# Kernel tuning notes

Measured on AMD Instinct MI355X. Metric: run time of the kernel, lower is better.

Reference implementation:

```python
import jax, jax.numpy as jnp
import numpy as np

N, E = 100000, 1600000
D_IN, D_H, D_OUT = 128, 256, 64


def _linear_params(k, fin, fout):
    b = 1.0 / np.sqrt(fin)
    k1, k2 = jax.random.split(k)
    W = jax.random.uniform(k1, (fout, fin), minval=-b, maxval=b, dtype=jnp.float32)
    bias = jax.random.uniform(k2, (fout,), minval=-b, maxval=b, dtype=jnp.float32)
    return W, bias


def setup_inputs() -> dict:
    key = jax.random.key(0)
    ks = jax.random.split(key, 10)
    x = jax.random.normal(ks[0], (N, D_IN), dtype=jnp.float32)
    row = jax.random.randint(ks[1], (E,), 0, N)
    col = jax.random.randint(ks[2], (E,), 0, N)
    vals = jax.random.uniform(ks[3], (E,), dtype=jnp.float32)
    W1a, b1a = _linear_params(ks[4], D_IN, D_H)
    W2a, b2a = _linear_params(ks[5], D_H, D_H)
    W1b, b1b = _linear_params(ks[6], D_H, D_H)
    W2b, b2b = _linear_params(ks[7], D_H, D_H)
    Wf1, bf1 = _linear_params(ks[8], D_H, D_H)
    Wf2, bf2 = _linear_params(ks[9], D_H, D_OUT)
    eps0 = jnp.zeros((1,), jnp.float32)
    eps1 = jnp.zeros((1,), jnp.float32)
    return {"x": x, "row": row, "col": col, "vals": vals,
            "eps0": eps0, "W1a": W1a, "b1a": b1a, "W2a": W2a, "b2a": b2a,
            "eps1": eps1, "W1b": W1b, "b1b": b1b, "W2b": W2b, "b2b": b2b,
            "Wf1": Wf1, "bf1": bf1, "Wf2": Wf2, "bf2": bf2}


def _spmm(row, col, vals, x):
    # y[i] = sum_j A[i,j] * x[j] over edges (row=i, col=j)
    msg = vals[:, None] * x[col]          # [E, d] gather
    return jax.ops.segment_sum(msg, row, num_segments=N)  # [N, d] scatter-add


def _gin_conv(x, row, col, vals, eps, W1, b1, W2, b2):
    y = _spmm(row, col, vals, x)
    h = y + (1.0 + eps) * x               # eps-residual (eps shape [1] broadcasts)
    h = jax.nn.relu(h @ W1.T + b1)
    return h @ W2.T + b2


def reference(x, row, col, vals, eps0, W1a, b1a, W2a, b2a,
              eps1, W1b, b1b, W2b, b2b, Wf1, bf1, Wf2, bf2):
    h = _gin_conv(x, row, col, vals, eps0, W1a, b1a, W2a, b2a)
    h = _gin_conv(h, row, col, vals, eps1, W1b, b1b, W2b, b2b)
    h = jax.nn.relu(h @ Wf1.T + bf1)
    # F.dropout with p=0 (default forward arg) is identity
    return h @ Wf2.T + bf2
```

## Files before the change

### kernel.cpp

```cpp
#include <hip/hip_runtime.h>
#include <cstdint>
#include <cstddef>


using h8  = __attribute__((ext_vector_type(8))) _Float16;
using us8 = __attribute__((ext_vector_type(8))) unsigned short;
using f4  = __attribute__((ext_vector_type(4))) float;

__device__ inline unsigned short f2h(float f) {
    _Float16 h = (_Float16)f;
    unsigned short u;
    __builtin_memcpy(&u, &h, 2);
    return u;
}

__device__ inline void wprep_body(const float* __restrict__ W,
                                  unsigned short* __restrict__ Wf,
                                  int K, int M, int idx) {
    int group = idx >> 9;
    int r     = idx & 511;
    int lane  = r >> 3;
    int j     = r & 7;
    int c  = group / (M / 16);
    int ct = group - c * (M / 16);
    int n = ct * 16 + (lane & 15);
    int k = c * 32 + (lane >> 4) * 8 + j;
    float w = W[(size_t)n * K + k];
    Wf[(size_t)group * 512 + (size_t)lane * 8 + j] = f2h(w);
}

__global__ __launch_bounds__(256) void k_prep0(
        const float* __restrict__ x, unsigned short* __restrict__ xh,
        int* __restrict__ cnt, int N, int ncv, int nzb,
        const float* W1a, unsigned short* Q1a, const float* W2a, unsigned short* Q2a,
        const float* W1b, unsigned short* Q1b, const float* W2b, unsigned short* Q2b,
        const float* Wf1, unsigned short* Qf1, const float* Wf2, unsigned short* Qf2) {
    int b = blockIdx.x;
    if (b < ncv) {
        int i = (b * 256 + threadIdx.x) * 4;
        float4 v = *(const float4*)(x + i);
        ushort4 o = {f2h(v.x), f2h(v.y), f2h(v.z), f2h(v.w)};
        *(ushort4*)(xh + i) = o;
        return;
    }
    b -= ncv;
    if (b < nzb) {
        int i = b * 256 + threadIdx.x;
        if (i < N) cnt[i] = 0;
        return;
    }
    b -= nzb;
    const float* W; unsigned short* Q; int K, M, lb;
    if      (b < 128)  { W = W1a; Q = Q1a; K = 128; M = 256; lb = b; }
    else if (b < 384)  { W = W2a; Q = Q2a; K = 256; M = 256; lb = b - 128; }
    else if (b < 640)  { W = W1b; Q = Q1b; K = 256; M = 256; lb = b - 384; }
    else if (b < 896)  { W = W2b; Q = Q2b; K = 256; M = 256; lb = b - 640; }
    else if (b < 1152) { W = Wf1; Q = Qf1; K = 256; M = 256; lb = b - 896; }
    else               { W = Wf2; Q = Qf2; K = 256; M = 64;  lb = b - 1152; }
    wprep_body(W, Q, K, M, lb * 256 + threadIdx.x);
}

__global__ __launch_bounds__(256) void k_scatter_d(const int* __restrict__ row,
                                                   const int* __restrict__ col,
                                                   const float* __restrict__ vals,
                                                   int* __restrict__ cnt,
                                                   int2* __restrict__ edges, int E) {
    int e = blockIdx.x * 256 + threadIdx.x;
    if (e < E) {
        int r = row[e];
        int p = atomicAdd(&cnt[r], 1);
        if (p < 64)
            edges[(size_t)r * 64 + p] = make_int2(col[e], __float_as_int(vals[e]));
    }
}

template <int DIN>
__device__ inline void gather_phase(const int* __restrict__ cnt,
                                    const int2* __restrict__ edges,
                                    const unsigned short* __restrict__ Xh,
                                    unsigned short* __restrict__ S,
                                    float scale, int r0, int wq, int lane,
                                    int lm, int N) {
    constexpr int L = DIN / 8;
    constexpr int R = 64 / L;
    constexpr int U = 8 / R;
    const int sub  = lane % L;
    const int part = lane / L;

    int nb = r0 + wq * 16 + lm;
    int cv = 0;
    if (nb < N) { cv = cnt[nb]; cv = cv < 64 ? cv : 64; }

    for (int j = 0; j < 16; ++j) {
        int n = r0 + wq * 16 + j;
        float acc[8];
#pragma unroll
        for (int k = 0; k < 8; ++k) acc[k] = 0.0f;
        bool valid = (n < N);
        if (valid) {
            int rem = __shfl(cv, j);
            if (rem > 0) {
                int s = n * 64;
                int idx = s + (lane < rem ? lane : 0);
                int2 ed = edges[idx];
                int   ci = ed.x;
                float vi = (lane < rem) ? __int_as_float(ed.y) : 0.0f;
                for (int jj = 0; jj < rem; jj += 8) {
                    int cc[U]; float vv[U];
#pragma unroll
                    for (int u = 0; u < U; ++u) {
                        int sl = jj + u * R + part;
                        cc[u] = __shfl(ci, sl);
                        vv[u] = __shfl(vi, sl);
                    }
                    h8 g[U];
#pragma unroll
                    for (int u = 0; u < U; ++u)
                        g[u] = *(const h8*)(Xh + (size_t)cc[u] * DIN + sub * 8);
#pragma unroll
                    for (int u = 0; u < U; ++u)
#pragma unroll
                        for (int k = 0; k < 8; ++k)
                            acc[k] = fmaf((float)g[u][k], vv[u], acc[k]);
                }
            }
#pragma unroll
            for (int st = L; st < 64; st <<= 1)
#pragma unroll
                for (int k = 0; k < 8; ++k)
                    acc[k] += __shfl_xor(acc[k], st);
        }
        if (part == 0) {
            us8 o;
            if (valid) {
                h8 xs = *(const h8*)(Xh + (size_t)n * DIN + sub * 8);
#pragma unroll
                for (int k = 0; k < 8; ++k)
                    o[k] = f2h(acc[k] + scale * (float)xs[k]);
            } else {
#pragma unroll
                for (int k = 0; k < 8; ++k) o[k] = 0;
            }
            int c = sub >> 2, q = sub & 3;
            unsigned off = (unsigned)(c * 2048 + wq * 512 + q * 128
                                      + ((j ^ (sub & 7)) * 8));
            *(us8*)(S + off) = o;
        }
    }
}

template <int DIN>
__global__ __launch_bounds__(256, 3) void k_conv(const int* __restrict__ cnt,
                                                 const int2* __restrict__ edges,
                                                 const unsigned short* __restrict__ Xh,
                                                 const unsigned short* __restrict__ Wq1,
                                                 const float* __restrict__ b1,
                                                 const unsigned short* __restrict__ Wq2,
                                                 const float* __restrict__ b2,
                                                 unsigned short* __restrict__ Cout,
                                                 const float* __restrict__ epsp,
                                                 int N) {
    constexpr int MH   = 256;
    constexpr int RT   = 4;
    constexpr int NCT1 = MH / 64;
    constexpr int NCH1 = DIN / 32;
    constexpr int NCH2 = MH / 32;
    constexpr int NCT2 = MH / 64;
    constexpr int HS   = 264;
    __shared__ unsigned short S[64 * HS];

    const int t    = threadIdx.x;
    const int lane = t & 63;
    const int wq   = t >> 6;
    const int r0   = blockIdx.x * 64;
    const int lm   = lane & 15;
    const int lq   = lane >> 4;
    const int kq   = lq * 8;

    const unsigned short* w1b = Wq1 + (size_t)(wq * NCT1) * 512 + (size_t)lane * 8;
    h8 wv[NCT1], wvn[NCT1];
#pragma unroll
    for (int ct = 0; ct < NCT1; ++ct)
        wv[ct] = *(const h8*)(w1b + ct * 512);

    gather_phase<DIN>(cnt, edges, Xh, S, 1.0f + epsp[0], r0, wq, lane, lm, N);
    __syncthreads();

    f4 acc[RT][NCT1];
#pragma unroll
    for (int rt = 0; rt < RT; ++rt)
#pragma unroll
        for (int ct = 0; ct < NCT1; ++ct) acc[rt][ct] = (f4){0.f, 0.f, 0.f, 0.f};

#pragma unroll
    for (int c = 0; c < NCH1; ++c) {
        if (c + 1 < NCH1) {
#pragma unroll
            for (int ct = 0; ct < NCT1; ++ct)
                wvn[ct] = *(const h8*)(w1b + ((size_t)(c + 1) * (MH / 16) + ct) * 512);
        }
        const int key = (4 * c + lq) & 7;
        h8 ah[RT];
#pragma unroll
        for (int rt = 0; rt < RT; ++rt)
            ah[rt] = *(const h8*)(S + c * 2048 + rt * 512 + lq * 128 + (lm ^ key) * 8);
#pragma unroll
        for (int ct = 0; ct < NCT1; ++ct)
#pragma unroll
            for (int rt = 0; rt < RT; ++rt)
                acc[rt][ct] = __builtin_amdgcn_mfma_f32_16x16x32_f16(ah[rt], wv[ct], acc[rt][ct], 0, 0, 0);
        if (c + 1 < NCH1) {
#pragma unroll
            for (int ct = 0; ct < NCT1; ++ct) wv[ct] = wvn[ct];
        }
    }
    __syncthreads();

#pragma unroll
    for (int ct = 0; ct < NCT1; ++ct) {
        const int col = wq * 64 + ct * 16 + lm;
        const float bv = b1[col];
#pragma unroll
        for (int rt = 0; rt < RT; ++rt) {
#pragma unroll
            for (int reg = 0; reg < 4; ++reg) {
                int rrow = rt * 16 + lq * 4 + reg;
                float v = acc[rt][ct][reg] + bv;
                v = v > 0.f ? v : 0.f;
                S[rrow * HS + col] = f2h(v);
            }
        }
    }

    const unsigned short* w2b = Wq2 + (size_t)(wq * NCT2) * 512 + (size_t)lane * 8;
    h8 wv2[NCT2], wv2n[NCT2];
#pragma unroll
    for (int ct = 0; ct < NCT2; ++ct)
        wv2[ct] = *(const h8*)(w2b + ct * 512);
    __syncthreads();

    f4 acc2[RT][NCT2];
#pragma unroll
    for (int rt = 0; rt < RT; ++rt)
#pragma unroll
        for (int ct = 0; ct < NCT2; ++ct) acc2[rt][ct] = (f4){0.f, 0.f, 0.f, 0.f};

#pragma unroll
    for (int c = 0; c < NCH2; ++c) {
        if (c + 1 < NCH2) {
#pragma unroll
            for (int ct = 0; ct < NCT2; ++ct)
                wv2n[ct] = *(const h8*)(w2b + ((size_t)(c + 1) * (MH / 16) + ct) * 512);
        }
        const int kk = c * 32 + kq;
        h8 hh[RT];
#pragma unroll
        for (int rt = 0; rt < RT; ++rt)
            hh[rt] = *(const h8*)(S + (rt * 16 + lm) * HS + kk);
#pragma unroll
        for (int ct = 0; ct < NCT2; ++ct)
#pragma unroll
            for (int rt = 0; rt < RT; ++rt)
                acc2[rt][ct] = __builtin_amdgcn_mfma_f32_16x16x32_f16(hh[rt], wv2[ct], acc2[rt][ct], 0, 0, 0);
        if (c + 1 < NCH2) {
#pragma unroll
            for (int ct = 0; ct < NCT2; ++ct) wv2[ct] = wv2n[ct];
        }
    }

#pragma unroll
    for (int ct = 0; ct < NCT2; ++ct) {
        const int col = wq * 64 + ct * 16 + lm;
        const float bv = b2[col];
#pragma unroll
        for (int rt = 0; rt < RT; ++rt) {
#pragma unroll
            for (int reg = 0; reg < 4; ++reg) {
                int n = r0 + rt * 16 + lq * 4 + reg;
                if (n < N)
                    Cout[(size_t)n * MH + col] = f2h(acc2[rt][ct][reg] + bv);
            }
        }
    }
}

__global__ __launch_bounds__(256, 3) void k_convh(const int* __restrict__ cnt,
                                                  const int2* __restrict__ edges,
                                                  const unsigned short* __restrict__ Xh,
                                                  const unsigned short* __restrict__ Wq1,
                                                  const float* __restrict__ b1,
                                                  const unsigned short* __restrict__ Wq2,
                                                  const float* __restrict__ b2,
                                                  const unsigned short* __restrict__ Wq3,
                                                  const float* __restrict__ b3,
                                                  const unsigned short* __restrict__ Wq4,
                                                  const float* __restrict__ b4,
                                                  float* __restrict__ outp,
                                                  const float* __restrict__ epsp,
                                                  int N) {
    constexpr int DIN  = 256;
    constexpr int MH   = 256;
    constexpr int RT   = 4;
    constexpr int NCT1 = 4;
    constexpr int NCH  = 8;
    constexpr int HS   = 264;
    __shared__ unsigned short S[64 * HS];

    const int t    = threadIdx.x;
    const int lane = t & 63;
    const int wq   = t >> 6;
    const int r0   = blockIdx.x * 64;
    const int lm   = lane & 15;
    const int lq   = lane >> 4;
    const int kq   = lq * 8;

    const unsigned short* w1b = Wq1 + (size_t)(wq * NCT1) * 512 + (size_t)lane * 8;
    h8 wv[NCT1], wvn[NCT1];
#pragma unroll
    for (int ct = 0; ct < NCT1; ++ct)
        wv[ct] = *(const h8*)(w1b + ct * 512);

    gather_phase<DIN>(cnt, edges, Xh, S, 1.0f + epsp[0], r0, wq, lane, lm, N);
    __syncthreads();

    f4 acc[RT][NCT1];
#pragma unroll
    for (int rt = 0; rt < RT; ++rt)
#pragma unroll
        for (int ct = 0; ct < NCT1; ++ct) acc[rt][ct] = (f4){0.f, 0.f, 0.f, 0.f};

#pragma unroll
    for (int c = 0; c < NCH; ++c) {
        if (c + 1 < NCH) {
#pragma unroll
            for (int ct = 0; ct < NCT1; ++ct)
                wvn[ct] = *(const h8*)(w1b + ((size_t)(c + 1) * (MH / 16) + ct) * 512);
        }
        const int key = (4 * c + lq) & 7;
        h8 ah[RT];
#pragma unroll
        for (int rt = 0; rt < RT; ++rt)
            ah[rt] = *(const h8*)(S + c * 2048 + rt * 512 + lq * 128 + (lm ^ key) * 8);
#pragma unroll
        for (int ct = 0; ct < NCT1; ++ct)
#pragma unroll
            for (int rt = 0; rt < RT; ++rt)
                acc[rt][ct] = __builtin_amdgcn_mfma_f32_16x16x32_f16(ah[rt], wv[ct], acc[rt][ct], 0, 0, 0);
        if (c + 1 < NCH) {
#pragma unroll
            for (int ct = 0; ct < NCT1; ++ct) wv[ct] = wvn[ct];
        }
    }
    __syncthreads();

#pragma unroll
    for (int ct = 0; ct < NCT1; ++ct) {
        const int col = wq * 64 + ct * 16 + lm;
        const float bv = b1[col];
#pragma unroll
        for (int rt = 0; rt < RT; ++rt) {
#pragma unroll
            for (int reg = 0; reg < 4; ++reg) {
                int rrow = rt * 16 + lq * 4 + reg;
                float v = acc[rt][ct][reg] + bv;
                v = v > 0.f ? v : 0.f;
                S[rrow * HS + col] = f2h(v);
            }
        }
    }

    const unsigned short* w2b = Wq2 + (size_t)(wq * NCT1) * 512 + (size_t)lane * 8;
    h8 wv2[NCT1], wv2n[NCT1];
#pragma unroll
    for (int ct = 0; ct < NCT1; ++ct)
        wv2[ct] = *(const h8*)(w2b + ct * 512);
    __syncthreads();

    f4 acc2[RT][NCT1];
#pragma unroll
    for (int rt = 0; rt < RT; ++rt)
#pragma unroll
        for (int ct = 0; ct < NCT1; ++ct) acc2[rt][ct] = (f4){0.f, 0.f, 0.f, 0.f};

#pragma unroll
    for (int c = 0; c < NCH; ++c) {
        if (c + 1 < NCH) {
#pragma unroll
            for (int ct = 0; ct < NCT1; ++ct)
                wv2n[ct] = *(const h8*)(w2b + ((size_t)(c + 1) * (MH / 16) + ct) * 512);
        }
        const int kk = c * 32 + kq;
        h8 hh[RT];
#pragma unroll
        for (int rt = 0; rt < RT; ++rt)
            hh[rt] = *(const h8*)(S + (rt * 16 + lm) * HS + kk);
#pragma unroll
        for (int ct = 0; ct < NCT1; ++ct)
#pragma unroll
            for (int rt = 0; rt < RT; ++rt)
                acc2[rt][ct] = __builtin_amdgcn_mfma_f32_16x16x32_f16(hh[rt], wv2[ct], acc2[rt][ct], 0, 0, 0);
        if (c + 1 < NCH) {
#pragma unroll
            for (int ct = 0; ct < NCT1; ++ct) wv2[ct] = wv2n[ct];
        }
    }
    __syncthreads();

#pragma unroll
    for (int ct = 0; ct < NCT1; ++ct) {
        const int col = wq * 64 + ct * 16 + lm;
        const float bv = b2[col];
#pragma unroll
        for (int rt = 0; rt < RT; ++rt) {
#pragma unroll
            for (int reg = 0; reg < 4; ++reg) {
                int rrow = rt * 16 + lq * 4 + reg;
                S[rrow * HS + col] = f2h(acc2[rt][ct][reg] + bv);
            }
        }
    }

    const unsigned short* w3b = Wq3 + (size_t)(wq * NCT1) * 512 + (size_t)lane * 8;
    h8 wv3[NCT1], wv3n[NCT1];
#pragma unroll
    for (int ct = 0; ct < NCT1; ++ct)
        wv3[ct] = *(const h8*)(w3b + ct * 512);
    __syncthreads();

    f4 acc3[RT][NCT1];
#pragma unroll
    for (int rt = 0; rt < RT; ++rt)
#pragma unroll
        for (int ct = 0; ct < NCT1; ++ct) acc3[rt][ct] = (f4){0.f, 0.f, 0.f, 0.f};

#pragma unroll
    for (int c = 0; c < NCH; ++c) {
        if (c + 1 < NCH) {
#pragma unroll
            for (int ct = 0; ct < NCT1; ++ct)
                wv3n[ct] = *(const h8*)(w3b + ((size_t)(c + 1) * (MH / 16) + ct) * 512);
        }
        const int kk = c * 32 + kq;
        h8 hh[RT];
#pragma unroll
        for (int rt = 0; rt < RT; ++rt)
            hh[rt] = *(const h8*)(S + (rt * 16 + lm) * HS + kk);
#pragma unroll
        for (int ct = 0; ct < NCT1; ++ct)
#pragma unroll
            for (int rt = 0; rt < RT; ++rt)
                acc3[rt][ct] = __builtin_amdgcn_mfma_f32_16x16x32_f16(hh[rt], wv3[ct], acc3[rt][ct], 0, 0, 0);
        if (c + 1 < NCH) {
#pragma unroll
            for (int ct = 0; ct < NCT1; ++ct) wv3[ct] = wv3n[ct];
        }
    }
    __syncthreads();

#pragma unroll
    for (int ct = 0; ct < NCT1; ++ct) {
        const int col = wq * 64 + ct * 16 + lm;
        const float bv = b3[col];
#pragma unroll
        for (int rt = 0; rt < RT; ++rt) {
#pragma unroll
            for (int reg = 0; reg < 4; ++reg) {
                int rrow = rt * 16 + lq * 4 + reg;
                float v = acc3[rt][ct][reg] + bv;
                v = v > 0.f ? v : 0.f;
                S[rrow * HS + col] = f2h(v);
            }
        }
    }

    const unsigned short* w4b = Wq4 + (size_t)wq * 512 + (size_t)lane * 8;
    h8 wv4 = *(const h8*)(w4b);
    h8 wv4n;
    __syncthreads();

    f4 acc4[RT];
#pragma unroll
    for (int rt = 0; rt < RT; ++rt) acc4[rt] = (f4){0.f, 0.f, 0.f, 0.f};

#pragma unroll
    for (int c = 0; c < NCH; ++c) {
        if (c + 1 < NCH)
            wv4n = *(const h8*)(w4b + (size_t)(c + 1) * 4 * 512);
        const int kk = c * 32 + kq;
        h8 hh[RT];
#pragma unroll
        for (int rt = 0; rt < RT; ++rt)
            hh[rt] = *(const h8*)(S + (rt * 16 + lm) * HS + kk);
#pragma unroll
        for (int rt = 0; rt < RT; ++rt)
            acc4[rt] = __builtin_amdgcn_mfma_f32_16x16x32_f16(hh[rt], wv4, acc4[rt], 0, 0, 0);
        if (c + 1 < NCH) wv4 = wv4n;
    }

    {
        const int col = wq * 16 + lm;
        const float bv = b4[col];
#pragma unroll
        for (int rt = 0; rt < RT; ++rt) {
#pragma unroll
            for (int reg = 0; reg < 4; ++reg) {
                int n = r0 + rt * 16 + lq * 4 + reg;
                if (n < N)
                    outp[(size_t)n * 64 + col] = acc4[rt][reg] + bv;
            }
        }
    }
}

extern "C" void kernel_launch(void* const* d_in, const int* in_sizes, int n_in,
                              void* d_out, int out_size, void* d_ws, size_t ws_size,
                              hipStream_t stream) {
    const float* x    = (const float*)d_in[0];
    const int*   row  = (const int*)d_in[1];
    const int*   col  = (const int*)d_in[2];
    const float* vals = (const float*)d_in[3];
    const float* eps0 = (const float*)d_in[4];
    const float* W1a  = (const float*)d_in[5];
    const float* b1a  = (const float*)d_in[6];
    const float* W2a  = (const float*)d_in[7];
    const float* b2a  = (const float*)d_in[8];
    const float* eps1 = (const float*)d_in[9];
    const float* W1b  = (const float*)d_in[10];
    const float* b1b  = (const float*)d_in[11];
    const float* W2b  = (const float*)d_in[12];
    const float* b2b  = (const float*)d_in[13];
    const float* Wf1  = (const float*)d_in[14];
    const float* bf1  = (const float*)d_in[15];
    const float* Wf2  = (const float*)d_in[16];
    const float* bf2  = (const float*)d_in[17];
    float* out = (float*)d_out;

    const int N = in_sizes[0] / 128;
    const int E = in_sizes[1];

    char* w = (char*)d_ws;
    auto alloc = [&](size_t bytes) -> void* {
        void* p = (void*)w;
        w += (bytes + 255) & ~(size_t)255;
        return p;
    };
    unsigned short* Hb1    = (unsigned short*)alloc((size_t)N * 256 * 2);
    unsigned short* xh     = (unsigned short*)alloc((size_t)N * 128 * 2);
    int*            cnt    = (int*)alloc((size_t)N * 4);
    int2*           edges  = (int2*)alloc((size_t)N * 64 * 8);
    unsigned short* Wq1a = (unsigned short*)alloc((size_t)128 * 256 * 2);
    unsigned short* Wq2a = (unsigned short*)alloc((size_t)256 * 256 * 2);
    unsigned short* Wq1b = (unsigned short*)alloc((size_t)256 * 256 * 2);
    unsigned short* Wq2b = (unsigned short*)alloc((size_t)256 * 256 * 2);
    unsigned short* Wqf1 = (unsigned short*)alloc((size_t)256 * 256 * 2);
    unsigned short* Wqf2 = (unsigned short*)alloc((size_t)256 * 64 * 2);

    const int ncv = (N * 128 / 4) / 256;
    const int nzb = (N + 255) / 256;
    k_prep0<<<ncv + nzb + 1216, 256, 0, stream>>>(
        x, xh, cnt, N, ncv, nzb,
        W1a, Wq1a, W2a, Wq2a, W1b, Wq1b, W2b, Wq2b, Wf1, Wqf1, Wf2, Wqf2);

    k_scatter_d<<<(E + 255) / 256, 256, 0, stream>>>(row, col, vals, cnt, edges, E);

    const int grid = (N + 63) / 64;

    k_conv<128><<<grid, 256, 0, stream>>>(cnt, edges, xh, Wq1a, b1a,
                                          Wq2a, b2a, Hb1, eps0, N);
    k_convh<<<grid, 256, 0, stream>>>(cnt, edges, Hb1, Wq1b, b1b,
                                      Wq2b, b2b, Wqf1, bf1, Wqf2, bf2,
                                      out, eps1, N);
}
```

Measured before the change: 515.3 us.

## Split gather from MLP into separate SpMM and MLP kernels with direct-to-LDS loads

Undoes the fusion of the neighbor gather and the MLP. A standalone SpMM kernel now runs one wave per node and writes the aggregated fp16 features to a global buffer Y. The MLP kernels then load their A tiles from Y straight into LDS using global_load_lds, replacing the swizzled LDS layout with a plain lane-ordered one. The aim is for the latency-bound gather to get full occupancy instead of being capped by the MLP's launch bounds and LDS use. In exchange there is an extra round trip of an N×D fp16 buffer through memory and two more kernel launches.

```diff
diff --git a/kernel.cpp b/kernel.cpp
--- a/kernel.cpp
+++ b/kernel.cpp
@@ -12,6 +12,12 @@
     unsigned short u;
     __builtin_memcpy(&u, &h, 2);
     return u;
+}
+
+__device__ inline void gl_lds16(const unsigned short* src, unsigned short* dst) {
+    __builtin_amdgcn_global_load_lds(
+        (const __attribute__((address_space(1))) unsigned int*)src,
+        (__attribute__((address_space(3))) unsigned int*)dst, 16, 0, 0);
 }
 
 __device__ inline void wprep_body(const float* __restrict__ W,
@@ -74,96 +80,82 @@
     }
 }
 
-template <int DIN>
-__device__ inline void gather_phase(const int* __restrict__ cnt,
-                                    const int2* __restrict__ edges,
-                                    const unsigned short* __restrict__ Xh,
-                                    unsigned short* __restrict__ S,
-                                    float scale, int r0, int wq, int lane,
-                                    int lm, int N) {
-    constexpr int L = DIN / 8;
+template <int D>
+__global__ __launch_bounds__(256) void k_spmm(const int* __restrict__ cnt,
+                                              const int2* __restrict__ edges,
+                                              const unsigned short* __restrict__ Xh,
+                                              unsigned short* __restrict__ Y,
+                                              const float* __restrict__ epsp,
+                                              int N) {
+    constexpr int L = D / 8;
     constexpr int R = 64 / L;
     constexpr int U = 8 / R;
+    int node = blockIdx.x * 4 + (threadIdx.x >> 6);
+    if (node >= N) return;
+    const int lane = threadIdx.x & 63;
     const int sub  = lane % L;
     const int part = lane / L;
-
-    int nb = r0 + wq * 16 + lm;
-    int cv = 0;
-    if (nb < N) { cv = cnt[nb]; cv = cv < 64 ? cv : 64; }
-
-    for (int j = 0; j < 16; ++j) {
-        int n = r0 + wq * 16 + j;
-        float acc[8];
-#pragma unroll
-        for (int k = 0; k < 8; ++k) acc[k] = 0.0f;
-        bool valid = (n < N);
-        if (valid) {
-            int rem = __shfl(cv, j);
-            if (rem > 0) {
-                int s = n * 64;
-                int idx = s + (lane < rem ? lane : 0);
-                int2 ed = edges[idx];
-                int   ci = ed.x;
-                float vi = (lane < rem) ? __int_as_float(ed.y) : 0.0f;
-                for (int jj = 0; jj < rem; jj += 8) {
-                    int cc[U]; float vv[U];
-#pragma unroll
-                    for (int u = 0; u < U; ++u) {
-                        int sl = jj + u * R + part;
-                        cc[u] = __shfl(ci, sl);
-                        vv[u] = __shfl(vi, sl);
-                    }
-                    h8 g[U];
-#pragma unroll
-                    for (int u = 0; u < U; ++u)
-                        g[u] = *(const h8*)(Xh + (size_t)cc[u] * DIN + sub * 8);
-#pragma unroll
-                    for (int u = 0; u < U; ++u)
-#pragma unroll
-                        for (int k = 0; k < 8; ++k)
-                            acc[k] = fmaf((float)g[u][k], vv[u], acc[k]);
-                }
-            }
-#pragma unroll
-            for (int st = L; st < 64; st <<= 1)
+    const float scale = 1.0f + epsp[0];
+
+    float acc[8];
+#pragma unroll
+    for (int k = 0; k < 8; ++k) acc[k] = 0.0f;
+
+    int rem = cnt[node];
+    rem = rem < 64 ? rem : 64;
+    if (rem > 0) {
+        int idx = node * 64 + (lane < rem ? lane : 0);
+        int2 ed = edges[idx];
+        int   ci = ed.x;
+        float vi = (lane < rem) ? __int_as_float(ed.y) : 0.0f;
+        for (int jj = 0; jj < rem; jj += 8) {
+            int cc[U]; float vv[U];
+#pragma unroll
+            for (int u = 0; u < U; ++u) {
+                int sl = jj + u * R + part;
+                cc[u] = __shfl(ci, sl);
+                vv[u] = __shfl(vi, sl);
+            }
+            h8 g[U];
+#pragma unroll
+            for (int u = 0; u < U; ++u)
+                g[u] = *(const h8*)(Xh + (size_t)cc[u] * D + sub * 8);
+#pragma unroll
+            for (int u = 0; u < U; ++u)
 #pragma unroll
                 for (int k = 0; k < 8; ++k)
-                    acc[k] += __shfl_xor(acc[k], st);
-        }
-        if (part == 0) {
-            us8 o;
-            if (valid) {
-                h8 xs = *(const h8*)(Xh + (size_t)n * DIN + sub * 8);
-#pragma unroll
-                for (int k = 0; k < 8; ++k)
-                    o[k] = f2h(acc[k] + scale * (float)xs[k]);
-            } else {
-#pragma unroll
-                for (int k = 0; k < 8; ++k) o[k] = 0;
-            }
-            int c = sub >> 2, q = sub & 3;
-            unsigned off = (unsigned)(c * 2048 + wq * 512 + q * 128
-                                      + ((j ^ (sub & 7)) * 8));
-            *(us8*)(S + off) = o;
-        }
-    }
-}
-
-template <int DIN>
-__global__ __launch_bounds__(256, 3) void k_conv(const int* __restrict__ cnt,
-                                                 const int2* __restrict__ edges,
-                                                 const unsigned short* __restrict__ Xh,
-                                                 const unsigned short* __restrict__ Wq1,
-                                                 const float* __restrict__ b1,
-                                                 const unsigned short* __restrict__ Wq2,
-                                                 const float* __restrict__ b2,
-                                                 unsigned short* __restrict__ Cout,
-                                                 const float* __restrict__ epsp,
-                                                 int N) {
+                    acc[k] = fmaf((float)g[u][k], vv[u], acc[k]);
+        }
+    }
+
+#pragma unroll
+    for (int st = L; st < 64; st <<= 1)
+#pragma unroll
+        for (int k = 0; k < 8; ++k)
+            acc[k] += __shfl_xor(acc[k], st);
+
+    if (part == 0) {
+        h8 xs = *(const h8*)(Xh + (size_t)node * D + sub * 8);
+        us8 o;
+#pragma unroll
+        for (int k = 0; k < 8; ++k)
+            o[k] = f2h(acc[k] + scale * (float)xs[k]);
+        *(us8*)(Y + (size_t)node * D + sub * 8) = o;
+    }
+}
+
+template <int K>
+__global__ __launch_bounds__(256, 3) void k_mlp(const unsigned short* __restrict__ A,
+                                                const unsigned short* __restrict__ Wq1,
+                                                const float* __restrict__ b1,
+                                                const unsigned short* __restrict__ Wq2,
+                                                const float* __restrict__ b2,
+                                                unsigned short* __restrict__ Cout,
+                                                int N) {
     constexpr int MH   = 256;
     constexpr int RT   = 4;
     constexpr int NCT1 = MH / 64;
-    constexpr int NCH1 = DIN / 32;
+    constexpr int NCH1 = K / 32;
     constexpr int NCH2 = MH / 32;
     constexpr int NCT2 = MH / 64;
     constexpr int HS   = 264;
@@ -177,13 +169,18 @@
     const int lq   = lane >> 4;
     const int kq   = lq * 8;
 
+    int gr = r0 + wq * 16 + lm;
+    if (gr >= N) gr = N - 1;
+    const unsigned short* gA = A + (size_t)gr * K + kq;
+
     const unsigned short* w1b = Wq1 + (size_t)(wq * NCT1) * 512 + (size_t)lane * 8;
     h8 wv[NCT1], wvn[NCT1];
 #pragma unroll
     for (int ct = 0; ct < NCT1; ++ct)
         wv[ct] = *(const h8*)(w1b + ct * 512);
-
-    gather_phase<DIN>(cnt, edges, Xh, S, 1.0f + epsp[0], r0, wq, lane, lm, N);
+#pragma unroll
+    for (int c = 0; c < NCH1; ++c)
+        gl_lds16(gA + c * 32, S + c * 2048 + wq * 512);
     __syncthreads();
 
     f4 acc[RT][NCT1];
@@ -199,11 +196,11 @@
             for (int ct = 0; ct < NCT1; ++ct)
                 wvn[ct] = *(const h8*)(w1b + ((size_t)(c + 1) * (MH / 16) + ct) * 512);
         }
-        const int key = (4 * c + lq) & 7;
+        const unsigned short* ab = S + c * 2048;
         h8 ah[RT];
 #pragma unroll
         for (int rt = 0; rt < RT; ++rt)
-            ah[rt] = *(const h8*)(S + c * 2048 + rt * 512 + lq * 128 + (lm ^ key) * 8);
+            ah[rt] = *(const h8*)(ab + rt * 512 + lane * 8);
 #pragma unroll
         for (int ct = 0; ct < NCT1; ++ct)
 #pragma unroll
@@ -271,7 +268,7 @@
 #pragma unroll
     for (int ct = 0; ct < NCT2; ++ct) {
         const int col = wq * 64 + ct * 16 + lm;
-        const float bv = b2[col];
+        const float bv = b2[ct * 16 + lm + wq * 64];
 #pragma unroll
         for (int rt = 0; rt < RT; ++rt) {
 #pragma unroll
@@ -284,9 +281,7 @@
     }
 }
 
-__global__ __launch_bounds__(256, 3) void k_convh(const int* __restrict__ cnt,
-                                                  const int2* __restrict__ edges,
-                                                  const unsigned short* __restrict__ Xh,
+__global__ __launch_bounds__(256, 3) void k_mlpbh(const unsigned short* __restrict__ A,
                                                   const unsigned short* __restrict__ Wq1,
                                                   const float* __restrict__ b1,
                                                   const unsigned short* __restrict__ Wq2,
@@ -296,9 +291,8 @@
                                                   const unsigned short* __restrict__ Wq4,
                                                   const float* __restrict__ b4,
                                                   float* __restrict__ outp,
-                                                  const float* __restrict__ epsp,
                                                   int N) {
-    constexpr int DIN  = 256;
+    constexpr int K    = 256;
     constexpr int MH   = 256;
     constexpr int RT   = 4;
     constexpr int NCT1 = 4;
@@ -314,13 +308,18 @@
     const int lq   = lane >> 4;
     const int kq   = lq * 8;
 
+    int gr = r0 + wq * 16 + lm;
+    if (gr >= N) gr = N - 1;
+    const unsigned short* gA = A + (size_t)gr * K + kq;
+
     const unsigned short* w1b = Wq1 + (size_t)(wq * NCT1) * 512 + (size_t)lane * 8;
     h8 wv[NCT1], wvn[NCT1];
 #pragma unroll
     for (int ct = 0; ct < NCT1; ++ct)
         wv[ct] = *(const h8*)(w1b + ct * 512);
-
-    gather_phase<DIN>(cnt, edges, Xh, S, 1.0f + epsp[0], r0, wq, lane, lm, N);
+#pragma unroll
+    for (int c = 0; c < NCH; ++c)
+        gl_lds16(gA + c * 32, S + c * 2048 + wq * 512);
     __syncthreads();
 
     f4 acc[RT][NCT1];
@@ -336,11 +335,11 @@
             for (int ct = 0; ct < NCT1; ++ct)
                 wvn[ct] = *(const h8*)(w1b + ((size_t)(c + 1) * (MH / 16) + ct) * 512);
         }
-        const int key = (4 * c + lq) & 7;
+        const unsigned short* ab = S + c * 2048;
         h8 ah[RT];
 #pragma unroll
         for (int rt = 0; rt < RT; ++rt)
-            ah[rt] = *(const h8*)(S + c * 2048 + rt * 512 + lq * 128 + (lm ^ key) * 8);
+            ah[rt] = *(const h8*)(ab + rt * 512 + lane * 8);
 #pragma unroll
         for (int ct = 0; ct < NCT1; ++ct)
 #pragma unroll
@@ -544,6 +543,7 @@
         w += (bytes + 255) & ~(size_t)255;
         return p;
     };
+    unsigned short* Y      = (unsigned short*)alloc((size_t)N * 256 * 2);
     unsigned short* Hb1    = (unsigned short*)alloc((size_t)N * 256 * 2);
     unsigned short* xh     = (unsigned short*)alloc((size_t)N * 128 * 2);
     int*            cnt    = (int*)alloc((size_t)N * 4);
@@ -563,11 +563,13 @@
 
     k_scatter_d<<<(E + 255) / 256, 256, 0, stream>>>(row, col, vals, cnt, edges, E);
 
-    const int grid = (N + 63) / 64;
-
-    k_conv<128><<<grid, 256, 0, stream>>>(cnt, edges, xh, Wq1a, b1a,
-                                          Wq2a, b2a, Hb1, eps0, N);
-    k_convh<<<grid, 256, 0, stream>>>(cnt, edges, Hb1, Wq1b, b1b,
-                                      Wq2b, b2b, Wqf1, bf1, Wqf2, bf2,
-                                      out, eps1, N);
-}
+    const int sgrid = (N + 3) / 4;
+    const int mgrid = (N + 63) / 64;
+
+    k_spmm<128><<<sgrid, 256, 0, stream>>>(cnt, edges, xh, Y, eps0, N);
+    k_mlp<128><<<mgrid, 256, 0, stream>>>(Y, Wq1a, b1a, Wq2a, b2a, Hb1, N);
+
+    k_spmm<256><<<sgrid, 256, 0, stream>>>(cnt, edges, Hb1, Y, eps1, N);
+    k_mlpbh<<<mgrid, 256, 0, stream>>>(Y, Wq1b, b1b, Wq2b, b2b,
+                                       Wqf1, bf1, Wqf2, bf2, out, N);
+}
```

After: 531.3 us. 1.03x slower.
